# Kernel optimization log

Hardware: AMD Instinct MI355X
Metric: run time of the kernel (lower is better)

## Reference

```python
import jax, jax.numpy as jnp
import numpy as np

B, T, U1, D, V = 4, 256, 65, 512, 1024

def setup_inputs() -> dict:
    key = jax.random.key(0)
    k1, k2, k3 = jax.random.split(key, 3)
    encoder_outputs = jax.random.normal(k1, (B, T, D), dtype=jnp.float32)
    decoder_outputs = jax.random.normal(k2, (B, U1, D), dtype=jnp.float32)
    # nn.Linear(2D, V, bias=False): weight shape (V, 2D), scaled like torch default init
    fc_weight = jax.random.normal(k3, (V, 2 * D), dtype=jnp.float32) * (1.0 / np.sqrt(2 * D))
    return {"encoder_outputs": encoder_outputs, "decoder_outputs": decoder_outputs, "fc_weight": fc_weight}

def reference(encoder_outputs, decoder_outputs, fc_weight):
    # Original: expand enc->(B,T,U,D), dec->(B,T,U,D), cat -> (B,T,U,2D), GELU(tanh), Linear.
    # Since GELU is elementwise and the linear has no bias, this equals two small
    # projections broadcast-added over the (T,U) grid (identical math, fused form).
    De = encoder_outputs.shape[-1]
    ge = jax.nn.gelu(encoder_outputs, approximate=True)  # (B,T,De)
    gd = jax.nn.gelu(decoder_outputs, approximate=True)  # (B,U,Dd)
    enc_proj = jnp.einsum('btd,vd->btv', ge, fc_weight[:, :De])  # (B,T,V)
    dec_proj = jnp.einsum('bud,vd->buv', gd, fc_weight[:, De:])  # (B,U,V)
    return enc_proj[:, :, None, :] + dec_proj[:, None, :, :]      # (B,T,U,V)
```

## Files before the change

kernel.cpp:

```cpp
#include <hip/hip_runtime.h>
#include <hip/hip_bf16.h>


#define B_ 4
#define T_ 256
#define U_ 65
#define D_ 512
#define V_ 1024
#define TB 4
#define USPLIT 8
#define ULEN 9

typedef __attribute__((ext_vector_type(8))) short bf16x8;
typedef __attribute__((ext_vector_type(4))) float f32x4;

__device__ __forceinline__ float gelu_tanh(float x) {
    const float c = 0.7978845608028654f;
    float x3 = x * x * x;
    float t = tanhf(c * (x + 0.044715f * x3));
    return 0.5f * x * (1.0f + t);
}

__device__ __forceinline__ ushort bf16bits(float x) {
    union { float f; unsigned u; } c; c.f = x;
    unsigned r = c.u + 0x7FFF + ((c.u >> 16) & 1);
    return (ushort)(r >> 16);
}

__global__ __launch_bounds__(256)
void prep_kernel(const float* __restrict__ enc,
                 const float* __restrict__ dec,
                 const float* __restrict__ W,
                 __hip_bfloat16* __restrict__ geB,
                 __hip_bfloat16* __restrict__ gdB,
                 __hip_bfloat16* __restrict__ WB) {
    const int NE4 = (B_ * T_ * D_) / 4;
    const int ND4 = (B_ * U_ * D_) / 4;
    const int NW4 = (V_ * 2 * D_) / 4;
    int i = blockIdx.x * blockDim.x + threadIdx.x;
    if (i < NE4) {
        float4 v = ((const float4*)enc)[i];
        ushort4 o;
        o.x = bf16bits(gelu_tanh(v.x));
        o.y = bf16bits(gelu_tanh(v.y));
        o.z = bf16bits(gelu_tanh(v.z));
        o.w = bf16bits(gelu_tanh(v.w));
        ((ushort4*)geB)[i] = o;
    } else if (i < NE4 + ND4) {
        int j = i - NE4;
        float4 v = ((const float4*)dec)[j];
        ushort4 o;
        o.x = bf16bits(gelu_tanh(v.x));
        o.y = bf16bits(gelu_tanh(v.y));
        o.z = bf16bits(gelu_tanh(v.z));
        o.w = bf16bits(gelu_tanh(v.w));
        ((ushort4*)gdB)[j] = o;
    } else if (i < NE4 + ND4 + NW4) {
        int j = i - NE4 - ND4;
        float4 v = ((const float4*)W)[j];
        ushort4 o;
        o.x = bf16bits(v.x);
        o.y = bf16bits(v.y);
        o.z = bf16bits(v.z);
        o.w = bf16bits(v.w);
        ((ushort4*)WB)[j] = o;
    }
}

__global__ __launch_bounds__(256)
void gemm_kernel(const __hip_bfloat16* __restrict__ geB,
                 const __hip_bfloat16* __restrict__ gdB,
                 const __hip_bfloat16* __restrict__ WB,
                 float* __restrict__ encP,
                 float* __restrict__ decP) {
    int blk = blockIdx.x;
    const __hip_bfloat16* A;
    float* C;
    int M, kofs, mt, nt;
    if (blk < 256) {
        A = geB; C = encP; M = B_ * T_; kofs = 0;
        mt = blk >> 4; nt = blk & 15;
    } else {
        blk -= 256;
        A = gdB; C = decP; M = B_ * U_; kofs = D_;
        mt = blk >> 4; nt = blk & 15;
    }
    const int lane = threadIdx.x & 63;
    const int w    = threadIdx.x >> 6;
    const int wr   = w >> 1, wc = w & 1;
    const int r16  = lane & 15;
    const int k8   = (lane >> 4) * 8;

    const int m_base = mt * 64 + wr * 32;
    const int n_base = nt * 64 + wc * 32;

    const __hip_bfloat16* Arow0 = A + (size_t)((m_base + 0  + r16) < M ? (m_base + 0  + r16) : 0) * D_ + k8;
    const __hip_bfloat16* Arow1 = A + (size_t)((m_base + 16 + r16) < M ? (m_base + 16 + r16) : 0) * D_ + k8;
    const __hip_bfloat16* Brow0 = WB + (size_t)(n_base + 0  + r16) * (2 * D_) + kofs + k8;
    const __hip_bfloat16* Brow1 = WB + (size_t)(n_base + 16 + r16) * (2 * D_) + kofs + k8;

    f32x4 acc[2][2] = {};
    bf16x8 aC0, aC1, bC0, bC1, aN0, aN1, bN0, bN1;

    aC0 = *(const bf16x8*)(Arow0);  aC1 = *(const bf16x8*)(Arow1);
    bC0 = *(const bf16x8*)(Brow0);  bC1 = *(const bf16x8*)(Brow1);

#pragma unroll 1
    for (int k0 = 0; k0 < D_; k0 += 64) {
        aN0 = *(const bf16x8*)(Arow0 + k0 + 32);
        aN1 = *(const bf16x8*)(Arow1 + k0 + 32);
        bN0 = *(const bf16x8*)(Brow0 + k0 + 32);
        bN1 = *(const bf16x8*)(Brow1 + k0 + 32);
        acc[0][0] = __builtin_amdgcn_mfma_f32_16x16x32_bf16(aC0, bC0, acc[0][0], 0, 0, 0);
        acc[0][1] = __builtin_amdgcn_mfma_f32_16x16x32_bf16(aC0, bC1, acc[0][1], 0, 0, 0);
        acc[1][0] = __builtin_amdgcn_mfma_f32_16x16x32_bf16(aC1, bC0, acc[1][0], 0, 0, 0);
        acc[1][1] = __builtin_amdgcn_mfma_f32_16x16x32_bf16(aC1, bC1, acc[1][1], 0, 0, 0);
        if (k0 + 64 < D_) {
            aC0 = *(const bf16x8*)(Arow0 + k0 + 64);
            aC1 = *(const bf16x8*)(Arow1 + k0 + 64);
            bC0 = *(const bf16x8*)(Brow0 + k0 + 64);
            bC1 = *(const bf16x8*)(Brow1 + k0 + 64);
        }
        acc[0][0] = __builtin_amdgcn_mfma_f32_16x16x32_bf16(aN0, bN0, acc[0][0], 0, 0, 0);
        acc[0][1] = __builtin_amdgcn_mfma_f32_16x16x32_bf16(aN0, bN1, acc[0][1], 0, 0, 0);
        acc[1][0] = __builtin_amdgcn_mfma_f32_16x16x32_bf16(aN1, bN0, acc[1][0], 0, 0, 0);
        acc[1][1] = __builtin_amdgcn_mfma_f32_16x16x32_bf16(aN1, bN1, acc[1][1], 0, 0, 0);
    }

    const int c_row0 = (lane >> 4) * 4;
#pragma unroll
    for (int mi = 0; mi < 2; ++mi) {
#pragma unroll
        for (int j = 0; j < 4; ++j) {
            int row = m_base + mi * 16 + c_row0 + j;
            if (row < M) {
#pragma unroll
                for (int ni = 0; ni < 2; ++ni) {
                    int col = n_base + ni * 16 + r16;
                    C[(size_t)row * V_ + col] = acc[mi][ni][j];
                }
            }
        }
    }
}

__global__ __launch_bounds__(256)
void bcast_kernel(const float* __restrict__ encP,
                  const float* __restrict__ decP,
                  float* __restrict__ out) {
    const int tid = threadIdx.x;
    const int bt0 = blockIdx.x * TB;
    const int b   = bt0 >> 8;
    const int u0  = blockIdx.y * ULEN;
    const int u1  = (u0 + ULEN < U_) ? u0 + ULEN : U_;

    f32x4 ev[TB];
#pragma unroll
    for (int i = 0; i < TB; ++i)
        ev[i] = ((const f32x4*)(encP + (size_t)(bt0 + i) * V_))[tid];

    const f32x4* d4 = (const f32x4*)(decP + (size_t)b * U_ * V_);
    f32x4* o4 = (f32x4*)(out + (size_t)bt0 * U_ * V_);

    for (int u = u0; u < u1; ++u) {
        f32x4 dv = d4[(size_t)u * (V_ / 4) + tid];
#pragma unroll
        for (int i = 0; i < TB; ++i) {
            f32x4 ov = ev[i] + dv;
            __builtin_nontemporal_store(ov, &o4[((size_t)i * U_ + u) * (V_ / 4) + tid]);
        }
    }
}

extern "C" void kernel_launch(void* const* d_in, const int* in_sizes, int n_in,
                              void* d_out, int out_size, void* d_ws, size_t ws_size,
                              hipStream_t stream) {
    const float* enc = (const float*)d_in[0];
    const float* dec = (const float*)d_in[1];
    const float* W   = (const float*)d_in[2];
    float* out = (float*)d_out;

    char* ws = (char*)d_ws;
    __hip_bfloat16* geB  = (__hip_bfloat16*)(ws);
    __hip_bfloat16* gdB  = (__hip_bfloat16*)(ws + 0x100000);
    __hip_bfloat16* WB   = (__hip_bfloat16*)(ws + 0x180000);
    float*          encP = (float*)(ws + 0x380000);
    float*          decP = (float*)(ws + 0x780000);

    const int total4 = (B_ * T_ * D_ + B_ * U_ * D_ + V_ * 2 * D_) / 4;
    prep_kernel<<<(total4 + 255) / 256, 256, 0, stream>>>(enc, dec, W, geB, gdB, WB);
    gemm_kernel<<<256 + 80, 256, 0, stream>>>(geB, gdB, WB, encP, decP);
    dim3 bgrid(T_ * B_ / TB, USPLIT);
    bcast_kernel<<<bgrid, 256, 0, stream>>>(encP, decP, out);
}
```

Before: 82.15 us.

## Retile broadcast kernel over V slices with decoder rows staged in LDS

The broadcast-add kernel now tiles by 8 (b,t) rows and a 128-wide V slice instead of 4 rows and a U range. Each block stages that V slice of all 65 decoder rows in shared memory and reuses it across its 8 rows. Each thread then streams 65 nontemporal stores along u for one row. The aim is to cut repeated global reads of decoder projections. In exchange, each thread's store addresses now stride by V along u, which may hurt write coalescing, and each block uses about 33KB of LDS, which may limit occupancy.

```diff
diff --git a/kernel.cpp b/kernel.cpp
--- a/kernel.cpp
+++ b/kernel.cpp
@@ -7,9 +7,8 @@
 #define U_ 65
 #define D_ 512
 #define V_ 1024
-#define TB 4
-#define USPLIT 8
-#define ULEN 9
+#define TBB 8
+#define VSL 128
 
 typedef __attribute__((ext_vector_type(8))) short bf16x8;
 typedef __attribute__((ext_vector_type(4))) float f32x4;
@@ -148,27 +147,29 @@
 void bcast_kernel(const float* __restrict__ encP,
                   const float* __restrict__ decP,
                   float* __restrict__ out) {
-    const int tid = threadIdx.x;
-    const int bt0 = blockIdx.x * TB;
-    const int b   = bt0 >> 8;
-    const int u0  = blockIdx.y * ULEN;
-    const int u1  = (u0 + ULEN < U_) ? u0 + ULEN : U_;
+    __shared__ float sdec[U_ * VSL];
+    const int t     = threadIdx.x;
+    const int bt0   = blockIdx.x * TBB;
+    const int b     = bt0 >> 8;
+    const int v0    = blockIdx.y * VSL;
+    const int i     = t >> 5;
+    const int c4    = t & 31;
 
-    f32x4 ev[TB];
-#pragma unroll
-    for (int i = 0; i < TB; ++i)
-        ev[i] = ((const f32x4*)(encP + (size_t)(bt0 + i) * V_))[tid];
+    f32x4 ev = *(const f32x4*)(encP + (size_t)(bt0 + i) * V_ + v0 + c4 * 4);
 
-    const f32x4* d4 = (const f32x4*)(decP + (size_t)b * U_ * V_);
-    f32x4* o4 = (f32x4*)(out + (size_t)bt0 * U_ * V_);
+    f32x4* sd4 = (f32x4*)sdec;
+    for (int j = t; j < U_ * (VSL / 4); j += 256) {
+        int u  = j >> 5;
+        int cc = j & 31;
+        sd4[j] = *(const f32x4*)(decP + (size_t)(b * U_ + u) * V_ + v0 + cc * 4);
+    }
+    __syncthreads();
 
-    for (int u = u0; u < u1; ++u) {
-        f32x4 dv = d4[(size_t)u * (V_ / 4) + tid];
-#pragma unroll
-        for (int i = 0; i < TB; ++i) {
-            f32x4 ov = ev[i] + dv;
-            __builtin_nontemporal_store(ov, &o4[((size_t)i * U_ + u) * (V_ / 4) + tid]);
-        }
+    float* orow = out + (size_t)(bt0 + i) * U_ * V_ + v0 + c4 * 4;
+    for (int u = 0; u < U_; ++u) {
+        f32x4 dv = sd4[u * (VSL / 4) + c4];
+        f32x4 ov = ev + dv;
+        __builtin_nontemporal_store(ov, (f32x4*)(orow + (size_t)u * V_));
     }
 }
 
@@ -190,6 +191,6 @@
     const int total4 = (B_ * T_ * D_ + B_ * U_ * D_ + V_ * 2 * D_) / 4;
     prep_kernel<<<(total4 + 255) / 256, 256, 0, stream>>>(enc, dec, W, geB, gdB, WB);
     gemm_kernel<<<256 + 80, 256, 0, stream>>>(geB, gdB, WB, encP, decP);
-    dim3 bgrid(T_ * B_ / TB, USPLIT);
+    dim3 bgrid((B_ * T_) / TBB, V_ / VSL);
     bcast_kernel<<<bgrid, 256, 0, stream>>>(encP, decP, out);
 }
```

Measured after the change: 108.0 us. 1.32x slower.
